# Performance work log

Hardware: AMD Instinct MI355X
Metric: run time of the kernel (lower is better)

Reference implementation:

```python
import jax, jax.numpy as jnp
import numpy as np

B, BS, WS = 2, 1024, 512
D_IN, H, DH, DFF = 2048, 16, 128, 8192
DM = H * DH


def _ln(x, g, eps=1e-5):
    m = x.mean(-1, keepdims=True)
    v = ((x - m) ** 2).mean(-1, keepdims=True)
    return (x - m) / jnp.sqrt(v + eps) * g


def _rotate_half(x):
    p = x.reshape(x.shape[:-1] + (-1, 2))
    a, b = p[..., 0], p[..., 1]
    return jnp.stack([-b, a], axis=-1).reshape(x.shape)


def _rope(x, freqs, scale):
    # xpos convention: align rotary table from the end for shorter sequences
    f = freqs[-x.shape[1]:]
    s = scale[-x.shape[1]:]
    return x * jnp.cos(f) * s + _rotate_half(x) * jnp.sin(f) * s


def setup_inputs():
    key = jax.random.key(0)
    ks = jax.random.split(key, 12)
    def w(k, shape, s=0.02):
        return jax.random.normal(k, shape, dtype=jnp.float32) * s
    x = jax.random.normal(ks[0], (B, BS, D_IN), dtype=jnp.float32)
    cache_k = jnp.zeros((B, WS, DM), jnp.float32)  # first call: zero KV cache
    cache_v = jnp.zeros((B, WS, DM), jnp.float32)
    # rotary frequencies over concatenated length, interleaved pairs
    pos = jnp.arange(BS + WS, dtype=jnp.float32)
    inv = 1.0 / (10000.0 ** (jnp.arange(0, DM, 2, dtype=jnp.float32) / DM))
    rotary = jnp.repeat(pos[:, None] * inv[None, :], 2, axis=-1)  # [BS+WS, DM]
    xscale = jax.random.uniform(ks[1], (BS + WS, DM), jnp.float32, 0.8, 1.2)
    # sliding window mask: query i (abs pos WS+i) sees keys j with i < j <= i+WS
    i = np.arange(BS)[:, None]
    j = np.arange(BS + WS)[None, :]
    mask = jnp.asarray(((j > i) & (j <= i + WS)).astype(np.int32))
    return dict(
        x=x, cache_k=cache_k, cache_v=cache_v, rotary=rotary, xscale=xscale, mask=mask,
        g_in=jnp.ones((D_IN,), jnp.float32),
        Wq=w(ks[2], (DM, D_IN)), Wk=w(ks[3], (DM, D_IN)), Wv=w(ks[4], (DM, D_IN)),
        g_q=jnp.ones((DM,), jnp.float32), g_k=jnp.ones((DM,), jnp.float32),
        Wlq=w(ks[5], (DM, DM)), blq=jnp.zeros((DM,), jnp.float32),
        Wlk=w(ks[6], (DM, DM)), blk=jnp.zeros((DM,), jnp.float32),
        Wlv=w(ks[7], (DM, DM)), blv=jnp.zeros((DM,), jnp.float32),
        Wo=w(ks[8], (DM, DM)), bo=jnp.zeros((DM,), jnp.float32),
        g_ffn=jnp.ones((DM,), jnp.float32),
        W1=w(ks[9], (DFF, DM)), W2=w(ks[10], (D_IN, DFF)))


def reference(x, cache_k, cache_v, rotary, xscale, mask, g_in, Wq, Wk, Wv, g_q, g_k,
              Wlq, blq, Wlk, blk, Wlv, blv, Wo, bo, g_ffn, W1, W2):
    xn = _ln(x, g_in)
    q = _ln(xn @ Wq.T, g_q)            # [B, BS, DM]
    k = _ln(xn @ Wk.T, g_k)
    v = xn @ Wv.T
    k = jnp.concatenate([cache_k, k], axis=1)  # [B, WS+BS, DM]
    v = jnp.concatenate([cache_v, v], axis=1)
    q_r = _rope(q, rotary, xscale)
    k_r = _rope(k, rotary, 1.0 / xscale)
    def heads(t):
        return t.reshape(t.shape[0], -1, H, DH).transpose(0, 2, 1, 3)
    qh = heads(q_r @ Wlq.T + blq)      # [B, H, BS, DH]
    kh = heads(k_r @ Wlk.T + blk)      # [B, H, WS+BS, DH]
    vh = heads(v @ Wlv.T + blv)
    scores = jnp.einsum('bhqd,bhkd->bhqk', qh, kh) / jnp.float32(np.sqrt(DH))
    scores = jnp.where(mask == 0, jnp.float32(-1e9), scores)
    p = jax.nn.softmax(scores, axis=-1)
    o = jnp.einsum('bhqk,bhkd->bhqd', p, vh)
    o = o.transpose(0, 2, 1, 3).reshape(x.shape[0], -1, DM) @ Wo.T + bo
    return jax.nn.relu(_ln(o, g_ffn) @ W1.T) @ W2.T
```

## Files before the change

### kernel.cpp

```cpp
#include <hip/hip_runtime.h>

typedef unsigned short u16;
typedef __attribute__((ext_vector_type(8))) __bf16 bf16x8;
typedef __attribute__((ext_vector_type(4))) float f32x4;

__device__ __forceinline__ float b2f(u16 u) {
    unsigned int i = ((unsigned int)u) << 16;
    return __builtin_bit_cast(float, i);
}
__device__ __forceinline__ u16 f2b(float f) {
    unsigned int x = __builtin_bit_cast(unsigned int, f);
    x += 0x7fffu + ((x >> 16) & 1u);
    return (u16)(x >> 16);
}
__device__ __forceinline__ void gld_lds16(const void* g, void* l) {
    __builtin_amdgcn_global_load_lds(
        (const __attribute__((address_space(1))) unsigned int*)g,
        (__attribute__((address_space(3))) unsigned int*)l, 16, 0, 0);
}

__global__ __launch_bounds__(256) void cvt_f32_bf16(
    const float* __restrict__ in, u16* __restrict__ out, int n4)
{
    int i = blockIdx.x * 256 + threadIdx.x;
    if (i < n4) {
        float4 v = ((const float4*)in)[i];
        ushort4 o;
        o.x = f2b(v.x); o.y = f2b(v.y); o.z = f2b(v.z); o.w = f2b(v.w);
        ((ushort4*)out)[i] = o;
    }
}

enum { EP_BF16 = 0, EP_BF16_BIAS, EP_BF16_RELU, EP_BF16_KV, EP_BF16_BIAS_VT, EP_F32_OUT };

template <int MODE>
__global__ __launch_bounds__(256) void gemm_bt(
    const u16* __restrict__ A, const u16* __restrict__ W,
    const float* __restrict__ bias, void* __restrict__ out,
    int M, int N, int K)
{
    __shared__ u16 As[128 * 64];
    __shared__ u16 Bs[128 * 64];
    const int tid = threadIdx.x;
    const int row0 = blockIdx.y * 128, col0 = blockIdx.x * 128;
    const int wave = tid >> 6, lane = tid & 63, quad = lane >> 4, l16 = lane & 15;
    const int wm = (wave >> 1) * 64, wn = (wave & 1) * 64;

    f32x4 acc[4][4];
#pragma unroll
    for (int i = 0; i < 4; ++i)
#pragma unroll
        for (int j = 0; j < 4; ++j) acc[i][j] = (f32x4){0.f, 0.f, 0.f, 0.f};

    const char* Ab = (const char*)A + (size_t)row0 * K * 2;
    const char* Wb = (const char*)W + (size_t)col0 * K * 2;
    const size_t ldb = (size_t)K * 2;

    for (int k0 = 0; k0 < K; k0 += 64) {
#pragma unroll
        for (int r = 0; r < 4; ++r) {
            int o = r * 4096 + tid * 16;
            int trow = o >> 7, tcolb = o & 127;
            gld_lds16(Ab + (size_t)trow * ldb + (size_t)k0 * 2 + tcolb, (char*)As + o);
            gld_lds16(Wb + (size_t)trow * ldb + (size_t)k0 * 2 + tcolb, (char*)Bs + o);
        }
        __syncthreads();
#pragma unroll
        for (int ks = 0; ks < 2; ++ks) {
            bf16x8 af[4], bfr[4];
#pragma unroll
            for (int i = 0; i < 4; ++i)
                af[i] = *(const bf16x8*)(As + (wm + i * 16 + l16) * 64 + ks * 32 + quad * 8);
#pragma unroll
            for (int j = 0; j < 4; ++j)
                bfr[j] = *(const bf16x8*)(Bs + (wn + j * 16 + l16) * 64 + ks * 32 + quad * 8);
#pragma unroll
            for (int i = 0; i < 4; ++i)
#pragma unroll
                for (int j = 0; j < 4; ++j)
                    acc[i][j] = __builtin_amdgcn_mfma_f32_16x16x32_bf16(af[i], bfr[j], acc[i][j], 0, 0, 0);
        }
        __syncthreads();
    }

#pragma unroll
    for (int j = 0; j < 4; ++j) {
        int gcol = col0 + wn + j * 16 + l16;
        float bv = 0.f;
        if (MODE == EP_BF16_BIAS || MODE == EP_BF16_BIAS_VT) bv = bias[gcol];
#pragma unroll
        for (int i = 0; i < 4; ++i) {
            int growb = row0 + wm + i * 16 + quad * 4;
#pragma unroll
            for (int reg = 0; reg < 4; ++reg) {
                int grow = growb + reg;
                float v = acc[i][j][reg] + bv;
                if (MODE == EP_BF16_RELU) v = fmaxf(v, 0.f);
                if (MODE == EP_F32_OUT) {
                    ((float*)out)[(size_t)grow * N + gcol] = v;
                } else if (MODE == EP_BF16_KV) {
                    int b = grow >> 10, s = grow & 1023;
                    ((u16*)out)[((size_t)(b * 1536 + 512 + s)) * N + gcol] = f2b(v);
                } else if (MODE == EP_BF16_BIAS_VT) {
                    int b = (grow >= 1536) ? 1 : 0;
                    int jk = grow - b * 1536;
                    ((u16*)out)[((size_t)(b * 2048 + gcol)) * 1536 + jk] = f2b(v);
                } else {
                    ((u16*)out)[(size_t)grow * N + gcol] = f2b(v);
                }
            }
        }
    }
}

template <int IN_F32>
__global__ __launch_bounds__(256) void ln_rows(
    const void* __restrict__ in, const float* __restrict__ gamma,
    u16* __restrict__ out)
{
    const int row = blockIdx.x, tid = threadIdx.x;
    const float* inf = (const float*)in + (size_t)row * 2048;
    const u16* inb = (const u16*)in + (size_t)row * 2048;
    float v[8], s1 = 0.f, s2 = 0.f;
#pragma unroll
    for (int i = 0; i < 8; ++i) {
        int c = tid + i * 256;
        float x = IN_F32 ? inf[c] : b2f(inb[c]);
        v[i] = x; s1 += x; s2 += x * x;
    }
#pragma unroll
    for (int off = 32; off >= 1; off >>= 1) { s1 += __shfl_xor(s1, off, 64); s2 += __shfl_xor(s2, off, 64); }
    __shared__ float ra[4], rb[4];
    int wave = tid >> 6, lane = tid & 63;
    if (lane == 0) { ra[wave] = s1; rb[wave] = s2; }
    __syncthreads();
    s1 = ra[0] + ra[1] + ra[2] + ra[3];
    s2 = rb[0] + rb[1] + rb[2] + rb[3];
    float mean = s1 * (1.f / 2048.f);
    float var = s2 * (1.f / 2048.f) - mean * mean;
    float rstd = rsqrtf(var + 1e-5f);
#pragma unroll
    for (int i = 0; i < 8; ++i) {
        int c = tid + i * 256;
        out[(size_t)row * 2048 + c] = f2b((v[i] - mean) * rstd * gamma[c]);
    }
}

__global__ __launch_bounds__(256) void qk_post(
    const u16* __restrict__ qpre, const u16* __restrict__ kpre,
    const float* __restrict__ gq, const float* __restrict__ gk,
    const float* __restrict__ rotary, const float* __restrict__ xscale,
    u16* __restrict__ qrope, u16* __restrict__ kfull)
{
    const int is_k = blockIdx.x & 1;
    const int row = blockIdx.x >> 1;
    const int b = row >> 10, s = row & 1023;
    const int tid = threadIdx.x, base = tid * 8;
    const u16* in = (is_k ? kpre : qpre) + (size_t)row * 2048;
    float v[8], s1 = 0.f, s2 = 0.f;
#pragma unroll
    for (int i = 0; i < 8; ++i) { float x = b2f(in[base + i]); v[i] = x; s1 += x; s2 += x * x; }
#pragma unroll
    for (int off = 32; off >= 1; off >>= 1) { s1 += __shfl_xor(s1, off, 64); s2 += __shfl_xor(s2, off, 64); }
    __shared__ float ra[4], rb[4];
    int wave = tid >> 6, lane = tid & 63;
    if (lane == 0) { ra[wave] = s1; rb[wave] = s2; }
    __syncthreads();
    s1 = ra[0] + ra[1] + ra[2] + ra[3];
    s2 = rb[0] + rb[1] + rb[2] + rb[3];
    float mean = s1 * (1.f / 2048.f);
    float rstd = rsqrtf(s2 * (1.f / 2048.f) - mean * mean + 1e-5f);
    const float* g = is_k ? gk : gq;
    const int rr = 512 + s;
    u16* outp = is_k ? (kfull + ((size_t)(b * 1536 + 512 + s)) * 2048)
                     : (qrope + (size_t)row * 2048);
#pragma unroll
    for (int p = 0; p < 4; ++p) {
        int e0 = base + 2 * p, e1 = e0 + 1;
        float x0 = (v[2 * p] - mean) * rstd * g[e0];
        float x1 = (v[2 * p + 1] - mean) * rstd * g[e1];
        float f = rotary[(size_t)rr * 2048 + e0];
        float sn, cs; sincosf(f, &sn, &cs);
        float sc0 = xscale[(size_t)rr * 2048 + e0];
        float sc1 = xscale[(size_t)rr * 2048 + e1];
        if (is_k) { sc0 = 1.f / sc0; sc1 = 1.f / sc1; }
        outp[e0] = f2b((x0 * cs - x1 * sn) * sc0);
        outp[e1] = f2b((x1 * cs + x0 * sn) * sc1);
    }
}

__global__ __launch_bounds__(256) void cache_prep(
    const float* __restrict__ cache_k, const float* __restrict__ cache_v,
    const float* __restrict__ rotary, const float* __restrict__ xscale,
    u16* __restrict__ kfull, u16* __restrict__ vfull)
{
    const int row = blockIdx.x;
    const int b = row >> 9, j = row & 511;
    const int base = threadIdx.x * 8;
    const float* ck = cache_k + ((size_t)row) * 2048;
    const float* cv = cache_v + ((size_t)row) * 2048;
    u16* ko = kfull + ((size_t)(b * 1536 + j)) * 2048;
    u16* vo = vfull + ((size_t)(b * 1536 + j)) * 2048;
#pragma unroll
    for (int p = 0; p < 4; ++p) {
        int e0 = base + 2 * p, e1 = e0 + 1;
        float x0 = ck[e0], x1 = ck[e1];
        float f = rotary[(size_t)j * 2048 + e0];
        float sn, cs; sincosf(f, &sn, &cs);
        float sc0 = 1.f / xscale[(size_t)j * 2048 + e0];
        float sc1 = 1.f / xscale[(size_t)j * 2048 + e1];
        ko[e0] = f2b((x0 * cs - x1 * sn) * sc0);
        ko[e1] = f2b((x1 * cs + x0 * sn) * sc1);
        vo[e0] = f2b(cv[e0]); vo[e1] = f2b(cv[e1]);
    }
}

__global__ __launch_bounds__(256) void attn(
    const u16* __restrict__ qh, const u16* __restrict__ kh,
    const u16* __restrict__ vt, u16* __restrict__ o)
{
    __shared__ u16 Qs[16 * 128];
    __shared__ float Ss[16 * 544];
    __shared__ u16 Ps[16 * 544];
    __shared__ float Ls[16];
    const int qt = blockIdx.x, h = blockIdx.y, b = blockIdx.z;
    const int i0 = qt * 16;
    const int tid = threadIdx.x;
    const int wave = tid >> 6, lane = tid & 63, quad = lane >> 4, l16 = lane & 15;

    {
        int r = tid >> 4, seg = tid & 15;
        const u16* src = qh + ((size_t)(b * 1024 + i0 + r)) * 2048 + h * 128 + seg * 8;
        *(uint4*)(Qs + r * 128 + seg * 8) = *(const uint4*)src;
    }
    __syncthreads();

    const float sm = 0.08838834764831845f;
    for (int kt = wave; kt < 33; kt += 4) {
        int jb = i0 + kt * 16;
        const u16* krow = kh + ((size_t)(b * 1536 + jb + l16)) * 2048 + h * 128 + quad * 8;
        const u16* qrow = Qs + l16 * 128 + quad * 8;
        f32x4 sacc = (f32x4){0.f, 0.f, 0.f, 0.f};
#pragma unroll
        for (int st = 0; st < 4; ++st) {
            bf16x8 aq = *(const bf16x8*)(qrow + st * 32);
            bf16x8 bk = *(const bf16x8*)(krow + st * 32);
            sacc = __builtin_amdgcn_mfma_f32_16x16x32_bf16(aq, bk, sacc, 0, 0, 0);
        }
        int jj = jb + l16;
#pragma unroll
        for (int reg = 0; reg < 4; ++reg) {
            int qi = i0 + quad * 4 + reg;
            bool valid = (jj > qi) && (jj <= qi + 512);
            Ss[(quad * 4 + reg) * 544 + kt * 16 + l16] = valid ? sacc[reg] * sm : -1e9f;
        }
    }
    __syncthreads();

    {
        int g = tid >> 4, l = tid & 15;
        float m = -1e30f;
        for (int j = l; j < 528; j += 16) m = fmaxf(m, Ss[g * 544 + j]);
#pragma unroll
        for (int off = 8; off >= 1; off >>= 1) m = fmaxf(m, __shfl_xor(m, off, 16));
        float sum = 0.f;
        for (int j = l; j < 528; j += 16) {
            float e = __expf(Ss[g * 544 + j] - m);
            sum += e;
            Ps[g * 544 + j] = f2b(e);
        }
        Ps[g * 544 + 528 + l] = 0;
#pragma unroll
        for (int off = 8; off >= 1; off >>= 1) sum += __shfl_xor(sum, off, 16);
        if (l == 0) Ls[g] = sum;
    }
    __syncthreads();

    f32x4 oa0 = (f32x4){0.f, 0.f, 0.f, 0.f}, oa1 = oa0;
    const u16* vbase = vt + ((size_t)(b * 2048 + h * 128 + wave * 32 + l16)) * 1536 + i0;
    for (int jc = 0; jc < 17; ++jc) {
        bf16x8 pf = *(const bf16x8*)(Ps + l16 * 544 + jc * 32 + quad * 8);
        bf16x8 v0 = *(const bf16x8*)(vbase + jc * 32 + quad * 8);
        bf16x8 v1 = *(const bf16x8*)(vbase + (size_t)16 * 1536 + jc * 32 + quad * 8);
        oa0 = __builtin_amdgcn_mfma_f32_16x16x32_bf16(pf, v0, oa0, 0, 0, 0);
        oa1 = __builtin_amdgcn_mfma_f32_16x16x32_bf16(pf, v1, oa1, 0, 0, 0);
    }
#pragma unroll
    for (int reg = 0; reg < 4; ++reg) {
        int q = quad * 4 + reg;
        float inv = 1.f / Ls[q];
        size_t orow = ((size_t)(b * 1024 + i0 + q)) * 2048 + h * 128 + wave * 32;
        o[orow + l16] = f2b(oa0[reg] * inv);
        o[orow + 16 + l16] = f2b(oa1[reg] * inv);
    }
}

extern "C" void kernel_launch(void* const* d_in, const int* in_sizes, int n_in,
                              void* d_out, int out_size, void* d_ws, size_t ws_size,
                              hipStream_t stream)
{
    const float* x       = (const float*)d_in[0];
    const float* cache_k = (const float*)d_in[1];
    const float* cache_v = (const float*)d_in[2];
    const float* rotary  = (const float*)d_in[3];
    const float* xscale  = (const float*)d_in[4];
    const float* g_in = (const float*)d_in[6];
    const float* Wq   = (const float*)d_in[7];
    const float* Wk   = (const float*)d_in[8];
    const float* Wv   = (const float*)d_in[9];
    const float* g_q  = (const float*)d_in[10];
    const float* g_k  = (const float*)d_in[11];
    const float* Wlq  = (const float*)d_in[12];
    const float* blq  = (const float*)d_in[13];
    const float* Wlk  = (const float*)d_in[14];
    const float* blk  = (const float*)d_in[15];
    const float* Wlv  = (const float*)d_in[16];
    const float* blv  = (const float*)d_in[17];
    const float* Wo   = (const float*)d_in[18];
    const float* bo   = (const float*)d_in[19];
    const float* g_ffn= (const float*)d_in[20];
    const float* W1   = (const float*)d_in[21];
    const float* W2   = (const float*)d_in[22];

    char* ws = (char*)d_ws;
    u16* xn    = (u16*)(ws + 0);
    u16* qpre  = (u16*)(ws + 8388608);
    u16* kpre  = (u16*)(ws + 16777216);
    u16* khb   = (u16*)(ws + 25165824);
    u16* vfull = (u16*)(ws + 37748736);
    u16* kfull = (u16*)(ws + 50331648);
    u16* vt    = (u16*)(ws + 62914560);
    u16* qrope = (u16*)(ws + 75563008);
    u16* h2    = (u16*)(ws + 83951616);
    u16* qhb   = qpre;
    u16* opre  = kpre;
    u16* obuf  = xn;
    u16* h1    = qrope;
    u16* wq_b  = (u16*)(ws + 25165824);
    u16* wk_b  = (u16*)(ws + 33554432);
    u16* wv_b  = (u16*)(ws + 50331648);
    u16* wlq_b = (u16*)(ws + 83951616);
    u16* wlk_b = (u16*)(ws + 92340224);
    u16* wlv_b = (u16*)(ws + 100728832);
    u16* wo_b  = (u16*)(ws + 25165824);
    u16* w1_b  = (u16*)(ws + 37748736);
    u16* w2_b  = (u16*)(ws + 37748736);

    const int N4M = 4194304 / 4;
    const int N16M = 16777216 / 4;

    ln_rows<1><<<2048, 256, 0, stream>>>(x, g_in, xn);
    cvt_f32_bf16<<<N4M / 256, 256, 0, stream>>>(Wq, wq_b, N4M);
    cvt_f32_bf16<<<N4M / 256, 256, 0, stream>>>(Wk, wk_b, N4M);
    cvt_f32_bf16<<<N4M / 256, 256, 0, stream>>>(Wv, wv_b, N4M);
    gemm_bt<EP_BF16><<<dim3(16, 16), 256, 0, stream>>>(xn, wq_b, nullptr, qpre, 2048, 2048, 2048);
    gemm_bt<EP_BF16><<<dim3(16, 16), 256, 0, stream>>>(xn, wk_b, nullptr, kpre, 2048, 2048, 2048);
    gemm_bt<EP_BF16_KV><<<dim3(16, 16), 256, 0, stream>>>(xn, wv_b, nullptr, vfull, 2048, 2048, 2048);
    cache_prep<<<1024, 256, 0, stream>>>(cache_k, cache_v, rotary, xscale, kfull, vfull);
    qk_post<<<4096, 256, 0, stream>>>(qpre, kpre, g_q, g_k, rotary, xscale, qrope, kfull);
    cvt_f32_bf16<<<N4M / 256, 256, 0, stream>>>(Wlq, wlq_b, N4M);
    cvt_f32_bf16<<<N4M / 256, 256, 0, stream>>>(Wlk, wlk_b, N4M);
    cvt_f32_bf16<<<N4M / 256, 256, 0, stream>>>(Wlv, wlv_b, N4M);
    gemm_bt<EP_BF16_BIAS><<<dim3(16, 16), 256, 0, stream>>>(qrope, wlq_b, blq, qhb, 2048, 2048, 2048);
    gemm_bt<EP_BF16_BIAS><<<dim3(16, 24), 256, 0, stream>>>(kfull, wlk_b, blk, khb, 3072, 2048, 2048);
    gemm_bt<EP_BF16_BIAS_VT><<<dim3(16, 24), 256, 0, stream>>>(vfull, wlv_b, blv, vt, 3072, 2048, 2048);
    attn<<<dim3(64, 16, 2), 256, 0, stream>>>(qhb, khb, vt, obuf);
    cvt_f32_bf16<<<N4M / 256, 256, 0, stream>>>(Wo, wo_b, N4M);
    gemm_bt<EP_BF16_BIAS><<<dim3(16, 16), 256, 0, stream>>>(obuf, wo_b, bo, opre, 2048, 2048, 2048);
    ln_rows<0><<<2048, 256, 0, stream>>>(opre, g_ffn, h1);
    cvt_f32_bf16<<<N16M / 256, 256, 0, stream>>>(W1, w1_b, N16M);
    gemm_bt<EP_BF16_RELU><<<dim3(64, 16), 256, 0, stream>>>(h1, w1_b, nullptr, h2, 2048, 8192, 2048);
    cvt_f32_bf16<<<N16M / 256, 256, 0, stream>>>(W2, w2_b, N16M);
    gemm_bt<EP_F32_OUT><<<dim3(16, 16), 256, 0, stream>>>(h2, w2_b, nullptr, d_out, 2048, 2048, 8192);
}
```

Baseline: 1.023 ms.

## Batch QKV and linear projections into grouped launches, split-K the Wo and W2 GEMMs

The three input projections and the three post-rope linear projections each become a single launch that uses blockIdx.z to select the problem, which fills more CUs per launch. The workspace layout is reshuffled so the converted weights for those grouped launches don't overlap. The Wo and W2 GEMMs switch to split-K with fp32 atomicAdd into zeroed buffers, giving more blocks on these 256-tile GEMMs. The cost is extra zeroing kernels, atomic traffic and non-deterministic summation order. The Wo output also becomes fp32 and is fed to the fp32 LayerNorm path.

```diff
diff --git a/kernel.cpp b/kernel.cpp
--- a/kernel.cpp
+++ b/kernel.cpp
@@ -29,6 +29,12 @@
         o.x = f2b(v.x); o.y = f2b(v.y); o.z = f2b(v.z); o.w = f2b(v.w);
         ((ushort4*)out)[i] = o;
     }
+}
+
+__global__ __launch_bounds__(256) void zero_f32(float* __restrict__ p, int n4)
+{
+    int i = blockIdx.x * 256 + threadIdx.x;
+    if (i < n4) ((float4*)p)[i] = (float4){0.f, 0.f, 0.f, 0.f};
 }
 
 enum { EP_BF16 = 0, EP_BF16_BIAS, EP_BF16_RELU, EP_BF16_KV, EP_BF16_BIAS_VT, EP_F32_OUT };
@@ -108,6 +114,152 @@
                 } else {
                     ((u16*)out)[(size_t)grow * N + gcol] = f2b(v);
                 }
+            }
+        }
+    }
+}
+
+struct FuseA { const u16* A; const u16* W; const float* bias; void* out; int M; int mode; };
+struct Fuse3 { FuseA z0, z1, z2; };
+
+__global__ __launch_bounds__(256) void gemm_bt_f(Fuse3 f, int K)
+{
+    FuseA p = (blockIdx.z == 0) ? f.z0 : ((blockIdx.z == 1) ? f.z1 : f.z2);
+    const int row0 = blockIdx.y * 128, col0 = blockIdx.x * 128;
+    if (row0 >= p.M) return;
+
+    __shared__ u16 As[128 * 64];
+    __shared__ u16 Bs[128 * 64];
+    const int tid = threadIdx.x;
+    const int wave = tid >> 6, lane = tid & 63, quad = lane >> 4, l16 = lane & 15;
+    const int wm = (wave >> 1) * 64, wn = (wave & 1) * 64;
+
+    f32x4 acc[4][4];
+#pragma unroll
+    for (int i = 0; i < 4; ++i)
+#pragma unroll
+        for (int j = 0; j < 4; ++j) acc[i][j] = (f32x4){0.f, 0.f, 0.f, 0.f};
+
+    const char* Ab = (const char*)p.A + (size_t)row0 * K * 2;
+    const char* Wb = (const char*)p.W + (size_t)col0 * K * 2;
+    const size_t ldb = (size_t)K * 2;
+
+    for (int k0 = 0; k0 < K; k0 += 64) {
+#pragma unroll
+        for (int r = 0; r < 4; ++r) {
+            int o = r * 4096 + tid * 16;
+            int trow = o >> 7, tcolb = o & 127;
+            gld_lds16(Ab + (size_t)trow * ldb + (size_t)k0 * 2 + tcolb, (char*)As + o);
+            gld_lds16(Wb + (size_t)trow * ldb + (size_t)k0 * 2 + tcolb, (char*)Bs + o);
+        }
+        __syncthreads();
+#pragma unroll
+        for (int ks = 0; ks < 2; ++ks) {
+            bf16x8 af[4], bfr[4];
+#pragma unroll
+            for (int i = 0; i < 4; ++i)
+                af[i] = *(const bf16x8*)(As + (wm + i * 16 + l16) * 64 + ks * 32 + quad * 8);
+#pragma unroll
+            for (int j = 0; j < 4; ++j)
+                bfr[j] = *(const bf16x8*)(Bs + (wn + j * 16 + l16) * 64 + ks * 32 + quad * 8);
+#pragma unroll
+            for (int i = 0; i < 4; ++i)
+#pragma unroll
+                for (int j = 0; j < 4; ++j)
+                    acc[i][j] = __builtin_amdgcn_mfma_f32_16x16x32_bf16(af[i], bfr[j], acc[i][j], 0, 0, 0);
+        }
+        __syncthreads();
+    }
+
+#pragma unroll
+    for (int j = 0; j < 4; ++j) {
+        int gcol = col0 + wn + j * 16 + l16;
+        float bv = (p.mode == EP_BF16_BIAS || p.mode == EP_BF16_BIAS_VT) ? p.bias[gcol] : 0.f;
+#pragma unroll
+        for (int i = 0; i < 4; ++i) {
+            int growb = row0 + wm + i * 16 + quad * 4;
+#pragma unroll
+            for (int reg = 0; reg < 4; ++reg) {
+                int grow = growb + reg;
+                u16 hv = f2b(acc[i][j][reg] + bv);
+                size_t idx;
+                if (p.mode == EP_BF16_KV) {
+                    int b = grow >> 10, s = grow & 1023;
+                    idx = ((size_t)(b * 1536 + 512 + s)) * 2048 + gcol;
+                } else if (p.mode == EP_BF16_BIAS_VT) {
+                    int b = (grow >= 1536) ? 1 : 0;
+                    int jk = grow - b * 1536;
+                    idx = ((size_t)(b * 2048 + gcol)) * 1536 + jk;
+                } else {
+                    idx = (size_t)grow * 2048 + gcol;
+                }
+                ((u16*)p.out)[idx] = hv;
+            }
+        }
+    }
+}
+
+__global__ __launch_bounds__(256) void gemm_bt_sk(
+    const u16* __restrict__ A, const u16* __restrict__ W,
+    const float* __restrict__ bias, float* __restrict__ out,
+    int N, int K, int Kc)
+{
+    __shared__ u16 As[128 * 64];
+    __shared__ u16 Bs[128 * 64];
+    const int tid = threadIdx.x;
+    const int row0 = blockIdx.y * 128, col0 = blockIdx.x * 128;
+    const int wave = tid >> 6, lane = tid & 63, quad = lane >> 4, l16 = lane & 15;
+    const int wm = (wave >> 1) * 64, wn = (wave & 1) * 64;
+    const int kbeg = blockIdx.z * Kc, kend = kbeg + Kc;
+
+    f32x4 acc[4][4];
+#pragma unroll
+    for (int i = 0; i < 4; ++i)
+#pragma unroll
+        for (int j = 0; j < 4; ++j) acc[i][j] = (f32x4){0.f, 0.f, 0.f, 0.f};
+
+    const char* Ab = (const char*)A + (size_t)row0 * K * 2;
+    const char* Wb = (const char*)W + (size_t)col0 * K * 2;
+    const size_t ldb = (size_t)K * 2;
+
+    for (int k0 = kbeg; k0 < kend; k0 += 64) {
+#pragma unroll
+        for (int r = 0; r < 4; ++r) {
+            int o = r * 4096 + tid * 16;
+            int trow = o >> 7, tcolb = o & 127;
+            gld_lds16(Ab + (size_t)trow * ldb + (size_t)k0 * 2 + tcolb, (char*)As + o);
+            gld_lds16(Wb + (size_t)trow * ldb + (size_t)k0 * 2 + tcolb, (char*)Bs + o);
+        }
+        __syncthreads();
+#pragma unroll
+        for (int ks = 0; ks < 2; ++ks) {
+            bf16x8 af[4], bfr[4];
+#pragma unroll
+            for (int i = 0; i < 4; ++i)
+                af[i] = *(const bf16x8*)(As + (wm + i * 16 + l16) * 64 + ks * 32 + quad * 8);
+#pragma unroll
+            for (int j = 0; j < 4; ++j)
+                bfr[j] = *(const bf16x8*)(Bs + (wn + j * 16 + l16) * 64 + ks * 32 + quad * 8);
+#pragma unroll
+            for (int i = 0; i < 4; ++i)
+#pragma unroll
+                for (int j = 0; j < 4; ++j)
+                    acc[i][j] = __builtin_amdgcn_mfma_f32_16x16x32_bf16(af[i], bfr[j], acc[i][j], 0, 0, 0);
+        }
+        __syncthreads();
+    }
+
+#pragma unroll
+    for (int j = 0; j < 4; ++j) {
+        int gcol = col0 + wn + j * 16 + l16;
+        float bv = (bias != nullptr && blockIdx.z == 0) ? bias[gcol] : 0.f;
+#pragma unroll
+        for (int i = 0; i < 4; ++i) {
+            int growb = row0 + wm + i * 16 + quad * 4;
+#pragma unroll
+            for (int reg = 0; reg < 4; ++reg) {
+                int grow = growb + reg;
+                atomicAdd(&out[(size_t)grow * N + gcol], acc[i][j][reg] + bv);
             }
         }
     }
@@ -323,53 +475,67 @@
     const float* W2   = (const float*)d_in[22];
 
     char* ws = (char*)d_ws;
-    u16* xn    = (u16*)(ws + 0);
-    u16* qpre  = (u16*)(ws + 8388608);
-    u16* kpre  = (u16*)(ws + 16777216);
-    u16* khb   = (u16*)(ws + 25165824);
-    u16* vfull = (u16*)(ws + 37748736);
-    u16* kfull = (u16*)(ws + 50331648);
-    u16* vt    = (u16*)(ws + 62914560);
-    u16* qrope = (u16*)(ws + 75563008);
-    u16* h2    = (u16*)(ws + 83951616);
-    u16* qhb   = qpre;
-    u16* opre  = kpre;
-    u16* obuf  = xn;
-    u16* h1    = qrope;
-    u16* wq_b  = (u16*)(ws + 25165824);
-    u16* wk_b  = (u16*)(ws + 33554432);
-    u16* wv_b  = (u16*)(ws + 50331648);
-    u16* wlq_b = (u16*)(ws + 83951616);
-    u16* wlk_b = (u16*)(ws + 92340224);
-    u16* wlv_b = (u16*)(ws + 100728832);
-    u16* wo_b  = (u16*)(ws + 25165824);
-    u16* w1_b  = (u16*)(ws + 37748736);
-    u16* w2_b  = (u16*)(ws + 37748736);
+    u16* xn     = (u16*)(ws + 0);
+    u16* qpre   = (u16*)(ws + 8388608);
+    u16* kpre   = (u16*)(ws + 16777216);
+    u16* wq_b   = (u16*)(ws + 25165824);
+    u16* khb    = (u16*)(ws + 25165824);
+    u16* vfull  = (u16*)(ws + 37748736);
+    u16* wv_b   = (u16*)(ws + 50331648);
+    u16* kfull  = (u16*)(ws + 50331648);
+    u16* wk_b   = (u16*)(ws + 62914560);
+    u16* vt     = (u16*)(ws + 62914560);
+    u16* qrope  = (u16*)(ws + 75563008);
+    u16* wlq_b  = (u16*)(ws + 83951616);
+    u16* wlk_b  = (u16*)(ws + 92340224);
+    u16* wlv_b  = (u16*)(ws + 100728832);
+    u16* h2     = (u16*)(ws + 83951616);
+    u16* qhb    = qpre;
+    u16* obuf   = xn;
+    u16* h1     = qrope;
+    float* opre32 = (float*)(ws + 8388608);
+    u16* wo_b   = (u16*)(ws + 25165824);
+    u16* w1_b   = (u16*)(ws + 37748736);
+    u16* w2_b   = (u16*)(ws + 37748736);
 
     const int N4M = 4194304 / 4;
     const int N16M = 16777216 / 4;
+    const int NZ4M = 4194304 / 4;
 
     ln_rows<1><<<2048, 256, 0, stream>>>(x, g_in, xn);
     cvt_f32_bf16<<<N4M / 256, 256, 0, stream>>>(Wq, wq_b, N4M);
     cvt_f32_bf16<<<N4M / 256, 256, 0, stream>>>(Wk, wk_b, N4M);
     cvt_f32_bf16<<<N4M / 256, 256, 0, stream>>>(Wv, wv_b, N4M);
-    gemm_bt<EP_BF16><<<dim3(16, 16), 256, 0, stream>>>(xn, wq_b, nullptr, qpre, 2048, 2048, 2048);
-    gemm_bt<EP_BF16><<<dim3(16, 16), 256, 0, stream>>>(xn, wk_b, nullptr, kpre, 2048, 2048, 2048);
-    gemm_bt<EP_BF16_KV><<<dim3(16, 16), 256, 0, stream>>>(xn, wv_b, nullptr, vfull, 2048, 2048, 2048);
+
+    Fuse3 fq;
+    fq.z0 = FuseA{xn, wq_b, nullptr, (void*)qpre,  2048, EP_BF16};
+    fq.z1 = FuseA{xn, wk_b, nullptr, (void*)kpre,  2048, EP_BF16};
+    fq.z2 = FuseA{xn, wv_b, nullptr, (void*)vfull, 2048, EP_BF16_KV};
+    gemm_bt_f<<<dim3(16, 16, 3), 256, 0, stream>>>(fq, 2048);
+
     cache_prep<<<1024, 256, 0, stream>>>(cache_k, cache_v, rotary, xscale, kfull, vfull);
     qk_post<<<4096, 256, 0, stream>>>(qpre, kpre, g_q, g_k, rotary, xscale, qrope, kfull);
     cvt_f32_bf16<<<N4M / 256, 256, 0, stream>>>(Wlq, wlq_b, N4M);
     cvt_f32_bf16<<<N4M / 256, 256, 0, stream>>>(Wlk, wlk_b, N4M);
     cvt_f32_bf16<<<N4M / 256, 256, 0, stream>>>(Wlv, wlv_b, N4M);
-    gemm_bt<EP_BF16_BIAS><<<dim3(16, 16), 256, 0, stream>>>(qrope, wlq_b, blq, qhb, 2048, 2048, 2048);
-    gemm_bt<EP_BF16_BIAS><<<dim3(16, 24), 256, 0, stream>>>(kfull, wlk_b, blk, khb, 3072, 2048, 2048);
-    gemm_bt<EP_BF16_BIAS_VT><<<dim3(16, 24), 256, 0, stream>>>(vfull, wlv_b, blv, vt, 3072, 2048, 2048);
+
+    Fuse3 fl;
+    fl.z0 = FuseA{qrope, wlq_b, blq, (void*)qhb, 2048, EP_BF16_BIAS};
+    fl.z1 = FuseA{kfull, wlk_b, blk, (void*)khb, 3072, EP_BF16_BIAS};
+    fl.z2 = FuseA{vfull, wlv_b, blv, (void*)vt,  3072, EP_BF16_BIAS_VT};
+    gemm_bt_f<<<dim3(16, 24, 3), 256, 0, stream>>>(fl, 2048);
+
     attn<<<dim3(64, 16, 2), 256, 0, stream>>>(qhb, khb, vt, obuf);
+
     cvt_f32_bf16<<<N4M / 256, 256, 0, stream>>>(Wo, wo_b, N4M);
-    gemm_bt<EP_BF16_BIAS><<<dim3(16, 16), 256, 0, stream>>>(obuf, wo_b, bo, opre, 2048, 2048, 2048);
-    ln_rows<0><<<2048, 256, 0, stream>>>(opre, g_ffn, h1);
+    zero_f32<<<NZ4M / 256, 256, 0, stream>>>(opre32, NZ4M);
+    gemm_bt_sk<<<dim3(16, 16, 2), 256, 0, stream>>>(obuf, wo_b, bo, opre32, 2048, 2048, 1024);
+    ln_rows<1><<<2048, 256, 0, stream>>>(opre32, g_ffn, h1);
+
     cvt_f32_bf16<<<N16M / 256, 256, 0, stream>>>(W1, w1_b, N16M);
     gemm_bt<EP_BF16_RELU><<<dim3(64, 16), 256, 0, stream>>>(h1, w1_b, nullptr, h2, 2048, 8192, 2048);
     cvt_f32_bf16<<<N16M / 256, 256, 0, stream>>>(W2, w2_b, N16M);
-    gemm_bt<EP_F32_OUT><<<dim3(16, 16), 256, 0, stream>>>(h2, w2_b, nullptr, d_out, 2048, 2048, 8192);
-}
+
+    zero_f32<<<NZ4M / 256, 256, 0, stream>>>((float*)d_out, NZ4M);
+    gemm_bt_sk<<<dim3(16, 16, 4), 256, 0, stream>>>(h2, w2_b, nullptr, (float*)d_out, 2048, 8192, 2048);
+}
```

After: 947.3 us. -7.4%, faster.

## Replace GEMM with 256x256 double-buffered 8-wave kernel, batched launches and split-K

Applied to the files above, without the earlier changes.

Replaces the 128x128 single-buffered GEMM with a 256x256-tile, 512-thread kernel. It double-buffers LDS, interleaves global-to-LDS staging with MFMA phases, and raises wave priority during MFMA. The Q/K/V and lq/lk/lv projections are each batched into one launch via a parameter array indexed by blockIdx.z. The Wo and W2 GEMMs use 4-way split-K: Wo writes four fp32 partials that a new LN kernel sums, and W2 accumulates into a zeroed output with atomics. The aim is more data reuse per tile, hidden load latency and better CU fill on the smaller GEMMs, at the cost of extra fp32 partial traffic, atomic contention and nondeterministic summation order.

```diff
diff --git a/kernel.cpp b/kernel.cpp
--- a/kernel.cpp
+++ b/kernel.cpp
@@ -31,82 +31,127 @@
     }
 }
 
-enum { EP_BF16 = 0, EP_BF16_BIAS, EP_BF16_RELU, EP_BF16_KV, EP_BF16_BIAS_VT, EP_F32_OUT };
-
-template <int MODE>
-__global__ __launch_bounds__(256) void gemm_bt(
-    const u16* __restrict__ A, const u16* __restrict__ W,
-    const float* __restrict__ bias, void* __restrict__ out,
-    int M, int N, int K)
-{
-    __shared__ u16 As[128 * 64];
-    __shared__ u16 Bs[128 * 64];
+__global__ __launch_bounds__(256) void zero_f32(float* __restrict__ p, int n4)
+{
+    int i = blockIdx.x * 256 + threadIdx.x;
+    if (i < n4) ((float4*)p)[i] = (float4){0.f, 0.f, 0.f, 0.f};
+}
+
+enum { EP_BF16 = 0, EP_BF16_BIAS, EP_BF16_RELU, EP_BF16_KV, EP_BF16_BIAS_VT,
+       EP_F32_OUT, EP_F32_ATOM };
+
+struct GZ { const u16* A; const u16* W; const float* bias; void* out;
+            int M, N, ldk, kbeg, Kc, mode; };
+struct GZ4 { GZ z[4]; };
+
+__global__ __launch_bounds__(512, 2) void gemm8p(GZ4 zz)
+{
+    __shared__ u16 L[2][2][2][256 * 32];
+    const GZ p = zz.z[blockIdx.z];
+    const int row0 = blockIdx.y * 256, col0 = blockIdx.x * 256;
+    if (row0 >= p.M) return;
+
     const int tid = threadIdx.x;
-    const int row0 = blockIdx.y * 128, col0 = blockIdx.x * 128;
-    const int wave = tid >> 6, lane = tid & 63, quad = lane >> 4, l16 = lane & 15;
-    const int wm = (wave >> 1) * 64, wn = (wave & 1) * 64;
-
-    f32x4 acc[4][4];
-#pragma unroll
-    for (int i = 0; i < 4; ++i)
+    const int w = tid >> 6, lane = tid & 63, quad = lane >> 4, l16 = lane & 15;
+    const int wr = w >> 2, wc = w & 3;
+    const int nt = p.Kc >> 6, niter = nt >> 1;
+
+    const u16* Ab = p.A + (size_t)row0 * p.ldk + p.kbeg;
+    const u16* Wb = p.W + (size_t)col0 * p.ldk + p.kbeg;
+    const int rl0 = lane >> 2;
+    const int g0 = lane & 3;
+
+    auto STAGE = [&](int m, int t, int kh) {
+        const u16* base = m ? Wb : Ab;
+        const int d = t & 1;
+#pragma unroll
+        for (int j = 0; j < 2; ++j) {
+            int blk = (w << 1) + j;
+            int rl = blk * 16 + rl0;
+            const u16* src = base + (size_t)rl * p.ldk + t * 64 + kh * 32 + g0 * 8;
+            gld_lds16(src, (u16*)&L[d][m][kh][0] + blk * 512);
+        }
+    };
+
+    f32x4 acc[8][4];
+#pragma unroll
+    for (int i = 0; i < 8; ++i)
 #pragma unroll
         for (int j = 0; j < 4; ++j) acc[i][j] = (f32x4){0.f, 0.f, 0.f, 0.f};
 
-    const char* Ab = (const char*)A + (size_t)row0 * K * 2;
-    const char* Wb = (const char*)W + (size_t)col0 * K * 2;
-    const size_t ldb = (size_t)K * 2;
-
-    for (int k0 = 0; k0 < K; k0 += 64) {
-#pragma unroll
-        for (int r = 0; r < 4; ++r) {
-            int o = r * 4096 + tid * 16;
-            int trow = o >> 7, tcolb = o & 127;
-            gld_lds16(Ab + (size_t)trow * ldb + (size_t)k0 * 2 + tcolb, (char*)As + o);
-            gld_lds16(Wb + (size_t)trow * ldb + (size_t)k0 * 2 + tcolb, (char*)Bs + o);
-        }
-        __syncthreads();
-#pragma unroll
-        for (int ks = 0; ks < 2; ++ks) {
-            bf16x8 af[4], bfr[4];
-#pragma unroll
-            for (int i = 0; i < 4; ++i)
-                af[i] = *(const bf16x8*)(As + (wm + i * 16 + l16) * 64 + ks * 32 + quad * 8);
-#pragma unroll
-            for (int j = 0; j < 4; ++j)
-                bfr[j] = *(const bf16x8*)(Bs + (wn + j * 16 + l16) * 64 + ks * 32 + quad * 8);
-#pragma unroll
-            for (int i = 0; i < 4; ++i)
-#pragma unroll
-                for (int j = 0; j < 4; ++j)
-                    acc[i][j] = __builtin_amdgcn_mfma_f32_16x16x32_bf16(af[i], bfr[j], acc[i][j], 0, 0, 0);
-        }
-        __syncthreads();
-    }
-
-#pragma unroll
-    for (int j = 0; j < 4; ++j) {
-        int gcol = col0 + wn + j * 16 + l16;
+    STAGE(0, 0, 0); STAGE(1, 0, 0); STAGE(0, 0, 1); STAGE(1, 0, 1);
+    STAGE(0, 1, 0); STAGE(1, 1, 0);
+    asm volatile("s_waitcnt vmcnt(4)" ::: "memory");
+    __builtin_amdgcn_s_barrier();
+
+    for (int i = 0; i < niter; ++i) {
+        const bool more = (i + 1 < niter);
+        const int T1 = 2 * i + 1, T2 = 2 * i + 2, T3 = 2 * i + 3;
+
+#define PHASE(D_, KH_, RH_, SM_, ST_, SKH_, SG_, VM_)                          \
+        {                                                                      \
+            bf16x8 af[4], bfv[4];                                              \
+            _Pragma("unroll")                                                  \
+            for (int f = 0; f < 4; ++f) {                                      \
+                af[f]  = *(const bf16x8*)&L[D_][0][KH_][(wr * 128 + RH_ * 64 + f * 16 + l16) * 32 + quad * 8]; \
+                bfv[f] = *(const bf16x8*)&L[D_][1][KH_][(wc * 64 + f * 16 + l16) * 32 + quad * 8]; \
+            }                                                                  \
+            if (SG_) STAGE(SM_, ST_, SKH_);                                    \
+            __builtin_amdgcn_s_barrier();                                      \
+            asm volatile("s_waitcnt lgkmcnt(0)" ::: "memory");                 \
+            __builtin_amdgcn_sched_barrier(0);                                 \
+            __builtin_amdgcn_s_setprio(1);                                     \
+            _Pragma("unroll")                                                  \
+            for (int fi = 0; fi < 4; ++fi)                                     \
+                _Pragma("unroll")                                              \
+                for (int fj = 0; fj < 4; ++fj)                                 \
+                    acc[RH_ * 4 + fi][fj] = __builtin_amdgcn_mfma_f32_16x16x32_bf16(af[fi], bfv[fj], acc[RH_ * 4 + fi][fj], 0, 0, 0); \
+            __builtin_amdgcn_s_setprio(0);                                     \
+            __builtin_amdgcn_sched_barrier(0);                                 \
+            VM_;                                                               \
+            __builtin_amdgcn_s_barrier();                                      \
+        }
+
+        PHASE(0, 0, 0, 0, T1, 1, true, );
+        PHASE(0, 0, 1, 1, T1, 1, true, );
+        PHASE(0, 1, 0, 0, T2, 0, more, );
+        PHASE(0, 1, 1, 1, T2, 0, more,
+              if (more) { asm volatile("s_waitcnt vmcnt(4)" ::: "memory"); }
+              else      { asm volatile("s_waitcnt vmcnt(0)" ::: "memory"); });
+        PHASE(1, 0, 0, 0, T2, 1, more, );
+        PHASE(1, 0, 1, 1, T2, 1, more, );
+        PHASE(1, 1, 0, 0, T3, 0, more, );
+        PHASE(1, 1, 1, 1, T3, 0, more,
+              if (more) { asm volatile("s_waitcnt vmcnt(4)" ::: "memory"); });
+#undef PHASE
+    }
+
+#pragma unroll
+    for (int fj = 0; fj < 4; ++fj) {
+        int gcol = col0 + wc * 64 + fj * 16 + l16;
         float bv = 0.f;
-        if (MODE == EP_BF16_BIAS || MODE == EP_BF16_BIAS_VT) bv = bias[gcol];
-#pragma unroll
-        for (int i = 0; i < 4; ++i) {
-            int growb = row0 + wm + i * 16 + quad * 4;
+        if (p.bias != nullptr) bv = p.bias[gcol];
+#pragma unroll
+        for (int ri = 0; ri < 8; ++ri) {
+            int growb = row0 + wr * 128 + ri * 16 + quad * 4;
 #pragma unroll
             for (int reg = 0; reg < 4; ++reg) {
-                int grow = growb + reg;
-                float v = acc[i][j][reg] + bv;
-                if (MODE == EP_BF16_RELU) v = fmaxf(v, 0.f);
-                if (MODE == EP_F32_OUT) {
-                    ((float*)out)[(size_t)grow * N + gcol] = v;
-                } else if (MODE == EP_BF16_KV) {
-                    int b = grow >> 10, s = grow & 1023;
-                    ((u16*)out)[((size_t)(b * 1536 + 512 + s)) * N + gcol] = f2b(v);
-                } else if (MODE == EP_BF16_BIAS_VT) {
-                    int b = (grow >= 1536) ? 1 : 0;
-                    int jk = grow - b * 1536;
-                    ((u16*)out)[((size_t)(b * 2048 + gcol)) * 1536 + jk] = f2b(v);
+                int gr = growb + reg;
+                float v = acc[ri][fj][reg] + bv;
+                if (p.mode == EP_BF16_RELU) v = fmaxf(v, 0.f);
+                if (p.mode == EP_F32_OUT) {
+                    ((float*)p.out)[(size_t)gr * p.N + gcol] = v;
+                } else if (p.mode == EP_F32_ATOM) {
+                    atomicAdd(&((float*)p.out)[(size_t)gr * p.N + gcol], v);
+                } else if (p.mode == EP_BF16_KV) {
+                    int b = gr >> 10, s = gr & 1023;
+                    ((u16*)p.out)[((size_t)(b * 1536 + 512 + s)) * 2048 + gcol] = f2b(v);
+                } else if (p.mode == EP_BF16_BIAS_VT) {
+                    int b = (gr >= 1536) ? 1 : 0;
+                    int jk = gr - b * 1536;
+                    ((u16*)p.out)[((size_t)(b * 2048 + gcol)) * 1536 + jk] = f2b(v);
                 } else {
-                    ((u16*)out)[(size_t)grow * N + gcol] = f2b(v);
+                    ((u16*)p.out)[(size_t)gr * p.N + gcol] = f2b(v);
                 }
             }
         }
@@ -143,6 +188,37 @@
     for (int i = 0; i < 8; ++i) {
         int c = tid + i * 256;
         out[(size_t)row * 2048 + c] = f2b((v[i] - mean) * rstd * gamma[c]);
+    }
+}
+
+__global__ __launch_bounds__(256) void ln4_rows(
+    const float* __restrict__ p0, const float* __restrict__ p1,
+    const float* __restrict__ p2, const float* __restrict__ p3,
+    const float* __restrict__ gamma, u16* __restrict__ out)
+{
+    const int row = blockIdx.x, tid = threadIdx.x;
+    const size_t rb_ = (size_t)row * 2048;
+    float v[8], s1 = 0.f, s2 = 0.f;
+#pragma unroll
+    for (int i = 0; i < 8; ++i) {
+        int c = tid + i * 256;
+        float x = p0[rb_ + c] + p1[rb_ + c] + p2[rb_ + c] + p3[rb_ + c];
+        v[i] = x; s1 += x; s2 += x * x;
+    }
+#pragma unroll
+    for (int off = 32; off >= 1; off >>= 1) { s1 += __shfl_xor(s1, off, 64); s2 += __shfl_xor(s2, off, 64); }
+    __shared__ float ra[4], rbs[4];
+    int wave = tid >> 6, lane = tid & 63;
+    if (lane == 0) { ra[wave] = s1; rbs[wave] = s2; }
+    __syncthreads();
+    s1 = ra[0] + ra[1] + ra[2] + ra[3];
+    s2 = rbs[0] + rbs[1] + rbs[2] + rbs[3];
+    float mean = s1 * (1.f / 2048.f);
+    float rstd = rsqrtf(s2 * (1.f / 2048.f) - mean * mean + 1e-5f);
+#pragma unroll
+    for (int i = 0; i < 8; ++i) {
+        int c = tid + i * 256;
+        out[rb_ + c] = f2b((v[i] - mean) * rstd * gamma[c]);
     }
 }
 
@@ -323,53 +399,94 @@
     const float* W2   = (const float*)d_in[22];
 
     char* ws = (char*)d_ws;
-    u16* xn    = (u16*)(ws + 0);
-    u16* qpre  = (u16*)(ws + 8388608);
-    u16* kpre  = (u16*)(ws + 16777216);
-    u16* khb   = (u16*)(ws + 25165824);
-    u16* vfull = (u16*)(ws + 37748736);
-    u16* kfull = (u16*)(ws + 50331648);
-    u16* vt    = (u16*)(ws + 62914560);
-    u16* qrope = (u16*)(ws + 75563008);
-    u16* h2    = (u16*)(ws + 83951616);
-    u16* qhb   = qpre;
-    u16* opre  = kpre;
-    u16* obuf  = xn;
-    u16* h1    = qrope;
-    u16* wq_b  = (u16*)(ws + 25165824);
-    u16* wk_b  = (u16*)(ws + 33554432);
-    u16* wv_b  = (u16*)(ws + 50331648);
-    u16* wlq_b = (u16*)(ws + 83951616);
-    u16* wlk_b = (u16*)(ws + 92340224);
-    u16* wlv_b = (u16*)(ws + 100728832);
-    u16* wo_b  = (u16*)(ws + 25165824);
-    u16* w1_b  = (u16*)(ws + 37748736);
-    u16* w2_b  = (u16*)(ws + 37748736);
+    u16* xn     = (u16*)(ws + 0);
+    u16* qpre   = (u16*)(ws + 8388608);
+    u16* kpre   = (u16*)(ws + 16777216);
+    u16* wq_b   = (u16*)(ws + 25165824);
+    u16* khb    = (u16*)(ws + 25165824);
+    u16* vfull  = (u16*)(ws + 37748736);
+    u16* wv_b   = (u16*)(ws + 50331648);
+    u16* kfull  = (u16*)(ws + 50331648);
+    u16* wk_b   = (u16*)(ws + 62914560);
+    u16* vt     = (u16*)(ws + 62914560);
+    u16* qrope  = (u16*)(ws + 75563008);
+    u16* wlq_b  = (u16*)(ws + 83951616);
+    u16* wlk_b  = (u16*)(ws + 92340224);
+    u16* wlv_b  = (u16*)(ws + 100728832);
+    u16* h2     = (u16*)(ws + 83951616);
+    u16* qhb    = qpre;
+    u16* obuf   = xn;
+    u16* h1     = (u16*)(ws + 0);
+    u16* wo_b   = (u16*)(ws + 25165824);
+    u16* w1_b   = (u16*)(ws + 37748736);
+    u16* w2_b   = (u16*)(ws + 37748736);
+    float* P0   = (float*)(ws + 8388608);
+    float* P1   = (float*)(ws + 33554432);
+    float* P2   = (float*)(ws + 50331648);
+    float* P3   = (float*)(ws + 67108864);
 
     const int N4M = 4194304 / 4;
     const int N16M = 16777216 / 4;
+    const int NZ4M = 4194304 / 4;
 
     ln_rows<1><<<2048, 256, 0, stream>>>(x, g_in, xn);
     cvt_f32_bf16<<<N4M / 256, 256, 0, stream>>>(Wq, wq_b, N4M);
     cvt_f32_bf16<<<N4M / 256, 256, 0, stream>>>(Wk, wk_b, N4M);
     cvt_f32_bf16<<<N4M / 256, 256, 0, stream>>>(Wv, wv_b, N4M);
-    gemm_bt<EP_BF16><<<dim3(16, 16), 256, 0, stream>>>(xn, wq_b, nullptr, qpre, 2048, 2048, 2048);
-    gemm_bt<EP_BF16><<<dim3(16, 16), 256, 0, stream>>>(xn, wk_b, nullptr, kpre, 2048, 2048, 2048);
-    gemm_bt<EP_BF16_KV><<<dim3(16, 16), 256, 0, stream>>>(xn, wv_b, nullptr, vfull, 2048, 2048, 2048);
+
+    {
+        GZ4 fq;
+        fq.z[0] = GZ{xn, wq_b, nullptr, (void*)qpre,  2048, 2048, 2048, 0, 2048, EP_BF16};
+        fq.z[1] = GZ{xn, wk_b, nullptr, (void*)kpre,  2048, 2048, 2048, 0, 2048, EP_BF16};
+        fq.z[2] = GZ{xn, wv_b, nullptr, (void*)vfull, 2048, 2048, 2048, 0, 2048, EP_BF16_KV};
+        fq.z[3] = fq.z[0];
+        gemm8p<<<dim3(8, 8, 3), 512, 0, stream>>>(fq);
+    }
+
     cache_prep<<<1024, 256, 0, stream>>>(cache_k, cache_v, rotary, xscale, kfull, vfull);
     qk_post<<<4096, 256, 0, stream>>>(qpre, kpre, g_q, g_k, rotary, xscale, qrope, kfull);
     cvt_f32_bf16<<<N4M / 256, 256, 0, stream>>>(Wlq, wlq_b, N4M);
     cvt_f32_bf16<<<N4M / 256, 256, 0, stream>>>(Wlk, wlk_b, N4M);
     cvt_f32_bf16<<<N4M / 256, 256, 0, stream>>>(Wlv, wlv_b, N4M);
-    gemm_bt<EP_BF16_BIAS><<<dim3(16, 16), 256, 0, stream>>>(qrope, wlq_b, blq, qhb, 2048, 2048, 2048);
-    gemm_bt<EP_BF16_BIAS><<<dim3(16, 24), 256, 0, stream>>>(kfull, wlk_b, blk, khb, 3072, 2048, 2048);
-    gemm_bt<EP_BF16_BIAS_VT><<<dim3(16, 24), 256, 0, stream>>>(vfull, wlv_b, blv, vt, 3072, 2048, 2048);
+
+    {
+        GZ4 fl;
+        fl.z[0] = GZ{qrope, wlq_b, blq, (void*)qhb, 2048, 2048, 2048, 0, 2048, EP_BF16_BIAS};
+        fl.z[1] = GZ{kfull, wlk_b, blk, (void*)khb, 3072, 2048, 2048, 0, 2048, EP_BF16_BIAS};
+        fl.z[2] = GZ{vfull, wlv_b, blv, (void*)vt,  3072, 2048, 2048, 0, 2048, EP_BF16_BIAS_VT};
+        fl.z[3] = fl.z[0];
+        gemm8p<<<dim3(8, 12, 3), 512, 0, stream>>>(fl);
+    }
+
     attn<<<dim3(64, 16, 2), 256, 0, stream>>>(qhb, khb, vt, obuf);
+
     cvt_f32_bf16<<<N4M / 256, 256, 0, stream>>>(Wo, wo_b, N4M);
-    gemm_bt<EP_BF16_BIAS><<<dim3(16, 16), 256, 0, stream>>>(obuf, wo_b, bo, opre, 2048, 2048, 2048);
-    ln_rows<0><<<2048, 256, 0, stream>>>(opre, g_ffn, h1);
+    {
+        GZ4 fo;
+        fo.z[0] = GZ{obuf, wo_b, bo,      (void*)P0, 2048, 2048, 2048, 0,    512, EP_F32_OUT};
+        fo.z[1] = GZ{obuf, wo_b, nullptr, (void*)P1, 2048, 2048, 2048, 512,  512, EP_F32_OUT};
+        fo.z[2] = GZ{obuf, wo_b, nullptr, (void*)P2, 2048, 2048, 2048, 1024, 512, EP_F32_OUT};
+        fo.z[3] = GZ{obuf, wo_b, nullptr, (void*)P3, 2048, 2048, 2048, 1536, 512, EP_F32_OUT};
+        gemm8p<<<dim3(8, 8, 4), 512, 0, stream>>>(fo);
+    }
+    ln4_rows<<<2048, 256, 0, stream>>>(P0, P1, P2, P3, g_ffn, h1);
+
     cvt_f32_bf16<<<N16M / 256, 256, 0, stream>>>(W1, w1_b, N16M);
-    gemm_bt<EP_BF16_RELU><<<dim3(64, 16), 256, 0, stream>>>(h1, w1_b, nullptr, h2, 2048, 8192, 2048);
+    {
+        GZ4 f1;
+        f1.z[0] = GZ{h1, w1_b, nullptr, (void*)h2, 2048, 8192, 2048, 0, 2048, EP_BF16_RELU};
+        f1.z[1] = f1.z[0]; f1.z[2] = f1.z[0]; f1.z[3] = f1.z[0];
+        gemm8p<<<dim3(32, 8, 1), 512, 0, stream>>>(f1);
+    }
+
     cvt_f32_bf16<<<N16M / 256, 256, 0, stream>>>(W2, w2_b, N16M);
-    gemm_bt<EP_F32_OUT><<<dim3(16, 16), 256, 0, stream>>>(h2, w2_b, nullptr, d_out, 2048, 2048, 8192);
-}
+    zero_f32<<<NZ4M / 256, 256, 0, stream>>>((float*)d_out, NZ4M);
+    {
+        GZ4 f2;
+        f2.z[0] = GZ{h2, w2_b, nullptr, d_out, 2048, 2048, 8192, 0,    2048, EP_F32_ATOM};
+        f2.z[1] = GZ{h2, w2_b, nullptr, d_out, 2048, 2048, 8192, 2048, 2048, EP_F32_ATOM};
+        f2.z[2] = GZ{h2, w2_b, nullptr, d_out, 2048, 2048, 8192, 4096, 2048, EP_F32_ATOM};
+        f2.z[3] = GZ{h2, w2_b, nullptr, d_out, 2048, 2048, 8192, 6144, 2048, EP_F32_ATOM};
+        gemm8p<<<dim3(8, 8, 4), 512, 0, stream>>>(f2);
+    }
+}
```

Result: faster. 950.7 us (-7.1%).
